# Kernel tuning notes

Measured on AMD Instinct MI355X. Metric: run time of the kernel, lower is better.

The kernel has to match this reference:

```python
import jax, jax.numpy as jnp
import numpy as np

B, NO, NR, D = 128, 256, 512, 1024


def setup_inputs() -> dict:
    key = jax.random.key(0)
    ks = jax.random.split(key, 8)
    obj_vecs = jax.random.normal(ks[0], (B, NO, D), dtype=jnp.float32)
    attr_vecs = jax.random.normal(ks[1], (B, NO, D), dtype=jnp.float32)
    rela_vecs = jax.random.normal(ks[2], (B, NR, D), dtype=jnp.float32)
    edges = jax.random.randint(ks[3], (B, NR, 2), 0, NO, dtype=jnp.int64)
    rela_masks = jnp.ones((B, NR, 1), dtype=jnp.float32)
    # Linear params (torch Linear: y = x @ W.T + b); store as [in, out]
    sa = 1.0 / np.sqrt(2 * D)
    sr = 1.0 / np.sqrt(3 * D)
    W_attr = jax.random.uniform(ks[4], (2 * D, D), jnp.float32, -sa, sa)
    b_attr = jax.random.uniform(ks[5], (D,), jnp.float32, -sa, sa)
    W_rela = jax.random.uniform(ks[6], (3 * D, D), jnp.float32, -sr, sr)
    b_rela = jax.random.uniform(ks[7], (D,), jnp.float32, -sr, sr)
    return {"obj_vecs": obj_vecs, "attr_vecs": attr_vecs, "rela_vecs": rela_vecs,
            "edges": edges, "rela_masks": rela_masks,
            "W_attr": W_attr, "b_attr": b_attr, "W_rela": W_rela, "b_rela": b_rela}


def reference(obj_vecs, attr_vecs, rela_vecs, edges, rela_masks,
              W_attr, b_attr, W_rela, b_rela):
    b, no, d = obj_vecs.shape
    nr = rela_vecs.shape[1]
    # feat_3d_to_2d: flatten batch, offset edge indices into the flat object table
    obj2 = obj_vecs.reshape(b * no, d)
    attr2 = attr_vecs.reshape(b * no, d)
    rela2 = rela_vecs.reshape(b * nr, d)
    offs = (jnp.arange(b, dtype=edges.dtype) * no)[:, None, None]  # [b,1,1]
    e2 = (edges + offs).reshape(b * nr, 2)

    # attribute branch: Linear(ReLU) on cat[obj, attr] + residual (dropout = eval/no-op)
    new_attr = jax.nn.relu(jnp.concatenate([obj2, attr2], axis=-1) @ W_attr + b_attr) + attr2

    # relation branch (rela_gnn_type == 0): gather subject/object, cat[s, rela, o]
    s_vecs = obj2[e2[:, 0]]  # [b*nr, d]
    o_vecs = obj2[e2[:, 1]]
    t_vecs = jnp.concatenate([s_vecs, rela2, o_vecs], axis=-1)  # [b*nr, 3d]
    new_rela = jax.nn.relu(t_vecs @ W_rela + b_rela) + rela2

    # feat_2d_to_3d: reshape back and apply relation mask
    new_obj3 = obj_vecs
    new_attr3 = new_attr.reshape(b, no, d)
    new_rela3 = new_rela.reshape(b, nr, d) * rela_masks
    return (new_obj3, new_attr3, new_rela3)
```

## Files before the change

kernel.cpp:

```cpp
#include <hip/hip_runtime.h>

#define B_   128
#define NO_  256
#define NR_  512
#define D_   1024

typedef __bf16 bf16x8 __attribute__((ext_vector_type(8)));
typedef float  f32x4  __attribute__((ext_vector_type(4)));

__device__ __forceinline__ unsigned short f2b(float f){
  unsigned int u = __float_as_uint(f);
  unsigned int r = (u + 0x7fffu + ((u >> 16) & 1u)) >> 16;
  return (unsigned short)r;
}

__global__ void conv_f32_bf16(const float4* __restrict__ in, uint4* __restrict__ out, int n8){
  int i = blockIdx.x * blockDim.x + threadIdx.x;
  if (i >= n8) return;
  float4 a = in[2*i], b = in[2*i+1];
  union { unsigned short s[8]; uint4 v; } p;
  p.s[0]=f2b(a.x); p.s[1]=f2b(a.y); p.s[2]=f2b(a.z); p.s[3]=f2b(a.w);
  p.s[4]=f2b(b.x); p.s[5]=f2b(b.y); p.s[6]=f2b(b.z); p.s[7]=f2b(b.w);
  out[i] = p.v;
}

__global__ void copy_vec4(const uint4* __restrict__ in, uint4* __restrict__ out, int n){
  int i = blockIdx.x * blockDim.x + threadIdx.x;
  if (i < n) out[i] = in[i];
}

__global__ void transpose_f32_bf16(const float* __restrict__ in,
                                   unsigned short* __restrict__ out, int R, int C){
  __shared__ unsigned short tile[32][33];
  int tx = threadIdx.x, ty = threadIdx.y;
  int x  = blockIdx.x * 32 + tx;
  int y0 = blockIdx.y * 32;
  #pragma unroll
  for (int i = 0; i < 4; i++) tile[ty + i*8][tx] = f2b(in[(size_t)(y0 + ty + i*8) * C + x]);
  __syncthreads();
  int ox  = y0 + tx;
  int oy0 = blockIdx.x * 32;
  #pragma unroll
  for (int i = 0; i < 4; i++) out[(size_t)(oy0 + ty + i*8) * R + ox] = tile[tx][ty + i*8];
}

template<int MODE>
__global__ void gemm_fused(const unsigned short* __restrict__ objb,
                           const unsigned short* __restrict__ xresb,
                           const float* __restrict__ xresf,
                           const int* __restrict__ edges,
                           const float* __restrict__ mask,
                           const unsigned short* __restrict__ WT,
                           const float* __restrict__ bias,
                           float* __restrict__ out)
{
  constexpr int K   = MODE ? 3*D_ : 2*D_;
  constexpr int LDA = 72;
  __shared__ unsigned short Asm[128*LDA];
  __shared__ unsigned short Bsm[128*LDA];

  const int t  = threadIdx.x;
  const int l  = t & 63;
  const int w  = t >> 6;
  const int wr = w >> 1, wc = w & 1;
  const int m0 = blockIdx.y * 128;
  const int n0 = blockIdx.x * 128;

  const int sr = t >> 3;
  const int sc = (t & 7) * 8;

  const unsigned short* pA0[4];
  const unsigned short* pA1[4];
  const unsigned short* pA2[4];
  #pragma unroll
  for (int i = 0; i < 4; i++){
    int m = m0 + i*32 + sr;
    if (MODE == 0){
      pA0[i] = objb  + (size_t)m * D_;
      pA1[i] = xresb + (size_t)m * D_;
      pA2[i] = nullptr;
    } else {
      int b = m >> 9;
      int s = edges[2*m];
      int o = edges[2*m + 1];
      pA0[i] = objb  + (size_t)((b << 8) + s) * D_;
      pA1[i] = xresb + (size_t)m * D_;
      pA2[i] = objb  + (size_t)((b << 8) + o) * D_;
    }
  }
  const unsigned short* pB[4];
  #pragma unroll
  for (int i = 0; i < 4; i++) pB[i] = WT + (size_t)(n0 + i*32 + sr) * K;

  f32x4 acc[4][4];
  #pragma unroll
  for (int x = 0; x < 4; x++)
    #pragma unroll
    for (int y = 0; y < 4; y++) acc[x][y] = (f32x4){0.f,0.f,0.f,0.f};

  const int kq = (l >> 4) * 8;
  const int fr = l & 15;

  for (int k0 = 0; k0 < K; k0 += 64){
    #pragma unroll
    for (int i = 0; i < 4; i++){
      const unsigned short* ga;
      if (MODE == 0){
        ga = (k0 < D_) ? pA0[i] + k0 : pA1[i] + (k0 - D_);
      } else {
        ga = (k0 < D_)   ? pA0[i] + k0
           : (k0 < 2*D_) ? pA1[i] + (k0 - D_)
           :               pA2[i] + (k0 - 2*D_);
      }
      *(uint4*)&Asm[(i*32 + sr) * LDA + sc] = *(const uint4*)(ga + sc);
      *(uint4*)&Bsm[(i*32 + sr) * LDA + sc] = *(const uint4*)(pB[i] + k0 + sc);
    }
    __syncthreads();

    #pragma unroll
    for (int ks = 0; ks < 2; ks++){
      bf16x8 af[4], bfv[4];
      #pragma unroll
      for (int x = 0; x < 4; x++)
        af[x]  = *(const bf16x8*)&Asm[(wr*64 + x*16 + fr) * LDA + ks*32 + kq];
      #pragma unroll
      for (int y = 0; y < 4; y++)
        bfv[y] = *(const bf16x8*)&Bsm[(wc*64 + y*16 + fr) * LDA + ks*32 + kq];
      #pragma unroll
      for (int x = 0; x < 4; x++)
        #pragma unroll
        for (int y = 0; y < 4; y++)
          acc[x][y] = __builtin_amdgcn_mfma_f32_16x16x32_bf16(af[x], bfv[y], acc[x][y], 0, 0, 0);
    }
    __syncthreads();
  }

  const int colb = n0 + wc*64 + fr;
  float bv[4];
  #pragma unroll
  for (int y = 0; y < 4; y++) bv[y] = bias[colb + y*16];

  const int rowb = m0 + wr*64 + ((l >> 4) << 2);
  #pragma unroll
  for (int x = 0; x < 4; x++){
    #pragma unroll
    for (int i = 0; i < 4; i++){
      int gr = rowb + x*16 + i;
      float mk = 1.f;
      if (MODE == 1) mk = mask[gr];
      size_t rbase = (size_t)gr * D_;
      #pragma unroll
      for (int y = 0; y < 4; y++){
        int gc = colb + y*16;
        float v = acc[x][y][i] + bv[y];
        v = fmaxf(v, 0.f) + xresf[rbase + gc];
        if (MODE == 1) v *= mk;
        out[rbase + gc] = v;
      }
    }
  }
}

extern "C" void kernel_launch(void* const* d_in, const int* in_sizes, int n_in,
                              void* d_out, int out_size, void* d_ws, size_t ws_size,
                              hipStream_t stream){
  const float* obj   = (const float*)d_in[0];
  const float* attr  = (const float*)d_in[1];
  const float* rela  = (const float*)d_in[2];
  const int*   edges = (const int*)d_in[3];
  const float* masks = (const float*)d_in[4];
  const float* Wa    = (const float*)d_in[5];
  const float* ba    = (const float*)d_in[6];
  const float* Wr    = (const float*)d_in[7];
  const float* br    = (const float*)d_in[8];

  const size_t NOBJ  = (size_t)B_*NO_*D_;
  const size_t NRELA = (size_t)B_*NR_*D_;

  float* out0 = (float*)d_out;
  float* out1 = out0 + NOBJ;
  float* out2 = out1 + NOBJ;

  unsigned short* objb  = (unsigned short*)d_out;
  unsigned short* attrb = objb + NOBJ;
  unsigned short* relab = (unsigned short*)(out1);
  unsigned short* WTa = (unsigned short*)d_ws;
  unsigned short* WTr = WTa + (size_t)1024*2048;

  conv_f32_bf16<<<(int)(NOBJ/8/256),  256, 0, stream>>>((const float4*)obj,  (uint4*)objb,  (int)(NOBJ/8));
  conv_f32_bf16<<<(int)(NOBJ/8/256),  256, 0, stream>>>((const float4*)attr, (uint4*)attrb, (int)(NOBJ/8));
  conv_f32_bf16<<<(int)(NRELA/8/256), 256, 0, stream>>>((const float4*)rela, (uint4*)relab, (int)(NRELA/8));

  transpose_f32_bf16<<<dim3(1024/32, 2048/32), dim3(32,8), 0, stream>>>(Wa, WTa, 2048, 1024);
  transpose_f32_bf16<<<dim3(1024/32, 3072/32), dim3(32,8), 0, stream>>>(Wr, WTr, 3072, 1024);

  gemm_fused<1><<<dim3(8, (B_*NR_)/128), 256, 0, stream>>>(objb, relab, rela, edges, masks, WTr, br, out2);
  gemm_fused<0><<<dim3(8, (B_*NO_)/128), 256, 0, stream>>>(objb, attrb, attr, nullptr, nullptr, WTa, ba, out1);

  int nv = (int)(NOBJ / 4);
  copy_vec4<<<nv/256, 256, 0, stream>>>((const uint4*)obj, (uint4*)out0, nv);
}
```

Measured before the change: 1.677 ms.

## Rewrite fused GEMM with 256x256 tiles, direct-to-LDS loads and double buffering

Measured after the change: 1.462 ms. 1.15x faster.

```diff
diff --git a/kernel.cpp b/kernel.cpp
--- a/kernel.cpp
+++ b/kernel.cpp
@@ -44,115 +44,181 @@
   for (int i = 0; i < 4; i++) out[(size_t)(oy0 + ty + i*8) * R + ox] = tile[tx][ty + i*8];
 }
 
+__device__ __forceinline__ void gload16(const void* g, void* l){
+  __builtin_amdgcn_global_load_lds((const __attribute__((address_space(1))) void*)g,
+                                   (__attribute__((address_space(3))) void*)l,
+                                   16, 0, 0);
+}
+
 template<int MODE>
-__global__ void gemm_fused(const unsigned short* __restrict__ objb,
-                           const unsigned short* __restrict__ xresb,
-                           const float* __restrict__ xresf,
-                           const int* __restrict__ edges,
-                           const float* __restrict__ mask,
-                           const unsigned short* __restrict__ WT,
-                           const float* __restrict__ bias,
-                           float* __restrict__ out)
+__global__ __launch_bounds__(512, 2)
+void gemm_fused(const unsigned short* __restrict__ objb,
+                const unsigned short* __restrict__ xresb,
+                const float* __restrict__ xresf,
+                const int* __restrict__ edges,
+                const float* __restrict__ mask,
+                const unsigned short* __restrict__ WT,
+                const float* __restrict__ bias,
+                float* __restrict__ out)
 {
-  constexpr int K   = MODE ? 3*D_ : 2*D_;
-  constexpr int LDA = 72;
-  __shared__ unsigned short Asm[128*LDA];
-  __shared__ unsigned short Bsm[128*LDA];
+  constexpr int K  = MODE ? 3*D_ : 2*D_;
+  constexpr int NT = K / 64;
+
+  __shared__ unsigned short Asm[2][2][128*64];
+  __shared__ unsigned short Bsm[2][2][128*64];
 
   const int t  = threadIdx.x;
   const int l  = t & 63;
   const int w  = t >> 6;
-  const int wr = w >> 1, wc = w & 1;
-  const int m0 = blockIdx.y * 128;
-  const int n0 = blockIdx.x * 128;
-
-  const int sr = t >> 3;
-  const int sc = (t & 7) * 8;
-
-  const unsigned short* pA0[4];
-  const unsigned short* pA1[4];
-  const unsigned short* pA2[4];
-  #pragma unroll
-  for (int i = 0; i < 4; i++){
-    int m = m0 + i*32 + sr;
-    if (MODE == 0){
-      pA0[i] = objb  + (size_t)m * D_;
-      pA1[i] = xresb + (size_t)m * D_;
-      pA2[i] = nullptr;
-    } else {
-      int b = m >> 9;
-      int s = edges[2*m];
-      int o = edges[2*m + 1];
-      pA0[i] = objb  + (size_t)((b << 8) + s) * D_;
-      pA1[i] = xresb + (size_t)m * D_;
-      pA2[i] = objb  + (size_t)((b << 8) + o) * D_;
+  const int wr = w >> 2;
+  const int wc = w & 3;
+
+  const int q8  = gridDim.x >> 3;
+  const int lin = (blockIdx.x & 7) * q8 + (blockIdx.x >> 3);
+  const int m0  = (lin >> 2) * 256;
+  const int n0  = (lin & 3) * 256;
+
+  const int trow = t >> 3;
+  const int gsl  = (((t & 7) ^ (trow & 7)) << 3);
+
+  unsigned int offA0[4], offA1[4], offA2[4], offB[4];
+  #pragma unroll
+  for (int h = 0; h < 2; h++){
+    #pragma unroll
+    for (int r = 0; r < 2; r++){
+      const int hr = h*2 + r;
+      const int m  = m0 + h*128 + r*64 + trow;
+      if (MODE == 0){
+        offA0[hr] = (unsigned)m * D_ + gsl;
+        offA1[hr] = offA0[hr];
+        offA2[hr] = 0;
+      } else {
+        const int b = m >> 9;
+        const int s = edges[2*m], o = edges[2*m+1];
+        offA0[hr] = (unsigned)((b << 8) + s) * D_ + gsl;
+        offA1[hr] = (unsigned)m * D_ + gsl;
+        offA2[hr] = (unsigned)((b << 8) + o) * D_ + gsl;
+      }
+      const int n = n0 + h*128 + r*64 + trow;
+      offB[hr] = (unsigned)n * K + gsl;
     }
   }
-  const unsigned short* pB[4];
-  #pragma unroll
-  for (int i = 0; i < 4; i++) pB[i] = WT + (size_t)(n0 + i*32 + sr) * K;
-
-  f32x4 acc[4][4];
-  #pragma unroll
-  for (int x = 0; x < 4; x++)
-    #pragma unroll
-    for (int y = 0; y < 4; y++) acc[x][y] = (f32x4){0.f,0.f,0.f,0.f};
-
-  const int kq = (l >> 4) * 8;
-  const int fr = l & 15;
-
-  for (int k0 = 0; k0 < K; k0 += 64){
-    #pragma unroll
-    for (int i = 0; i < 4; i++){
-      const unsigned short* ga;
-      if (MODE == 0){
-        ga = (k0 < D_) ? pA0[i] + k0 : pA1[i] + (k0 - D_);
-      } else {
-        ga = (k0 < D_)   ? pA0[i] + k0
-           : (k0 < 2*D_) ? pA1[i] + (k0 - D_)
-           :               pA2[i] + (k0 - 2*D_);
-      }
-      *(uint4*)&Asm[(i*32 + sr) * LDA + sc] = *(const uint4*)(ga + sc);
-      *(uint4*)&Bsm[(i*32 + sr) * LDA + sc] = *(const uint4*)(pB[i] + k0 + sc);
-    }
-    __syncthreads();
-
-    #pragma unroll
-    for (int ks = 0; ks < 2; ks++){
-      bf16x8 af[4], bfv[4];
-      #pragma unroll
-      for (int x = 0; x < 4; x++)
-        af[x]  = *(const bf16x8*)&Asm[(wr*64 + x*16 + fr) * LDA + ks*32 + kq];
-      #pragma unroll
-      for (int y = 0; y < 4; y++)
-        bfv[y] = *(const bf16x8*)&Bsm[(wc*64 + y*16 + fr) * LDA + ks*32 + kq];
-      #pragma unroll
-      for (int x = 0; x < 4; x++)
-        #pragma unroll
-        for (int y = 0; y < 4; y++)
-          acc[x][y] = __builtin_amdgcn_mfma_f32_16x16x32_bf16(af[x], bfv[y], acc[x][y], 0, 0, 0);
-    }
-    __syncthreads();
+
+#define STAGE_A(tile, half) do{                                               \
+    const int _tl = (tile); const int _k = _tl*64; const int _b = _tl & 1;    \
+    const unsigned short *_g0, *_g1;                                          \
+    if (MODE == 0){                                                           \
+      if (_k < D_){ _g0 = objb  + offA0[(half)*2+0] + _k;                     \
+                    _g1 = objb  + offA0[(half)*2+1] + _k; }                   \
+      else        { _g0 = xresb + offA1[(half)*2+0] + (_k - D_);              \
+                    _g1 = xresb + offA1[(half)*2+1] + (_k - D_); }            \
+    } else {                                                                  \
+      if (_k < D_){ _g0 = objb  + offA0[(half)*2+0] + _k;                     \
+                    _g1 = objb  + offA0[(half)*2+1] + _k; }                   \
+      else if (_k < 2*D_){ _g0 = xresb + offA1[(half)*2+0] + (_k - D_);       \
+                           _g1 = xresb + offA1[(half)*2+1] + (_k - D_); }     \
+      else        { _g0 = objb  + offA2[(half)*2+0] + (_k - 2*D_);            \
+                    _g1 = objb  + offA2[(half)*2+1] + (_k - 2*D_); }          \
+    }                                                                         \
+    gload16(_g0, &Asm[_b][half][(w*8     ) * 64]);                            \
+    gload16(_g1, &Asm[_b][half][(w*8 + 64) * 64]);                            \
+  }while(0)
+
+#define STAGE_B(tile, half) do{                                               \
+    const int _tl = (tile); const int _k = _tl*64; const int _b = _tl & 1;    \
+    gload16(WT + offB[(half)*2+0] + _k, &Bsm[_b][half][(w*8     ) * 64]);     \
+    gload16(WT + offB[(half)*2+1] + _k, &Bsm[_b][half][(w*8 + 64) * 64]);     \
+  }while(0)
+
+  f32x4 acc[8][4];
+  #pragma unroll
+  for (int X = 0; X < 8; X++)
+    #pragma unroll
+    for (int Y = 0; Y < 4; Y++) acc[X][Y] = (f32x4){0.f,0.f,0.f,0.f};
+
+  const int fr  = l & 15;
+  const int swz = (fr & 7) << 4;
+  const int rdo = (l >> 4) << 4;
+
+  auto lda = [&](int buf, int qm, int x, int kh) -> bf16x8 {
+    const int r = qm*64 + x*16 + fr;
+    return *(const bf16x8*)((const char*)&Asm[buf][wr][r*64] + ((kh*64 + rdo) ^ swz));
+  };
+  auto ldb = [&](int buf, int qn, int y, int kh) -> bf16x8 {
+    const int r = (wc & 1)*64 + qn*32 + y*16 + fr;
+    return *(const bf16x8*)((const char*)&Bsm[buf][wc>>1][r*64] + ((kh*64 + rdo) ^ swz));
+  };
+
+  bf16x8 af[4][2], bq0[2][2], bq1[2][2];
+
+#define MFMA16(qm, qn, BQ)                                                    \
+  __builtin_amdgcn_s_setprio(1);                                              \
+  _Pragma("unroll")                                                           \
+  for (int x = 0; x < 4; x++){                                                \
+    _Pragma("unroll")                                                         \
+    for (int y = 0; y < 2; y++){                                              \
+      acc[(qm)*4+x][(qn)*2+y] = __builtin_amdgcn_mfma_f32_16x16x32_bf16(      \
+          af[x][0], BQ[y][0], acc[(qm)*4+x][(qn)*2+y], 0, 0, 0);              \
+      acc[(qm)*4+x][(qn)*2+y] = __builtin_amdgcn_mfma_f32_16x16x32_bf16(      \
+          af[x][1], BQ[y][1], acc[(qm)*4+x][(qn)*2+y], 0, 0, 0);              \
+    }                                                                         \
+  }                                                                           \
+  __builtin_amdgcn_s_setprio(0);
+
+  STAGE_A(0,0); STAGE_A(0,1); STAGE_B(0,0); STAGE_B(0,1);
+  STAGE_A(1,0);
+  asm volatile("s_waitcnt vmcnt(2)" ::: "memory");
+  __builtin_amdgcn_s_barrier();
+
+  for (int tt = 0; tt < NT; ++tt){
+    const int cur = tt & 1;
+    #pragma unroll
+    for (int x = 0; x < 4; x++){ af[x][0] = lda(cur,0,x,0); af[x][1] = lda(cur,0,x,1); }
+    #pragma unroll
+    for (int y = 0; y < 2; y++){ bq0[y][0] = ldb(cur,0,y,0); bq0[y][1] = ldb(cur,0,y,1); }
+    if (tt+1 < NT) STAGE_A(tt+1, 1);
+    __builtin_amdgcn_s_barrier();
+    MFMA16(0,0,bq0)
+    __builtin_amdgcn_s_barrier();
+    #pragma unroll
+    for (int y = 0; y < 2; y++){ bq1[y][0] = ldb(cur,1,y,0); bq1[y][1] = ldb(cur,1,y,1); }
+    if (tt+1 < NT) STAGE_B(tt+1, 0);
+    __builtin_amdgcn_s_barrier();
+    MFMA16(0,1,bq1)
+    __builtin_amdgcn_s_barrier();
+    #pragma unroll
+    for (int x = 0; x < 4; x++){ af[x][0] = lda(cur,1,x,0); af[x][1] = lda(cur,1,x,1); }
+    if (tt+1 < NT) STAGE_B(tt+1, 1);
+    __builtin_amdgcn_s_barrier();
+    MFMA16(1,1,bq1)
+    __builtin_amdgcn_s_barrier();
+    if (tt+2 < NT) STAGE_A(tt+2, 0);
+    MFMA16(1,0,bq0)
+    asm volatile("s_waitcnt vmcnt(2)" ::: "memory");
+    __builtin_amdgcn_s_barrier();
   }
+#undef STAGE_A
+#undef STAGE_B
+#undef MFMA16
 
   const int colb = n0 + wc*64 + fr;
   float bv[4];
   #pragma unroll
-  for (int y = 0; y < 4; y++) bv[y] = bias[colb + y*16];
-
-  const int rowb = m0 + wr*64 + ((l >> 4) << 2);
-  #pragma unroll
-  for (int x = 0; x < 4; x++){
+  for (int Y = 0; Y < 4; Y++) bv[Y] = bias[colb + Y*16];
+
+  const int rowq = (l >> 4) << 2;
+  #pragma unroll
+  for (int X = 0; X < 8; X++){
     #pragma unroll
     for (int i = 0; i < 4; i++){
-      int gr = rowb + x*16 + i;
+      const int gr = m0 + wr*128 + X*16 + rowq + i;
       float mk = 1.f;
       if (MODE == 1) mk = mask[gr];
-      size_t rbase = (size_t)gr * D_;
+      const size_t rbase = (size_t)gr * D_;
       #pragma unroll
-      for (int y = 0; y < 4; y++){
-        int gc = colb + y*16;
-        float v = acc[x][y][i] + bv[y];
+      for (int Y = 0; Y < 4; Y++){
+        const int gc = colb + Y*16;
+        float v = acc[X][Y][i] + bv[Y];
         v = fmaxf(v, 0.f) + xresf[rbase + gc];
         if (MODE == 1) v *= mk;
         out[rbase + gc] = v;
@@ -194,8 +260,8 @@
   transpose_f32_bf16<<<dim3(1024/32, 2048/32), dim3(32,8), 0, stream>>>(Wa, WTa, 2048, 1024);
   transpose_f32_bf16<<<dim3(1024/32, 3072/32), dim3(32,8), 0, stream>>>(Wr, WTr, 3072, 1024);
 
-  gemm_fused<1><<<dim3(8, (B_*NR_)/128), 256, 0, stream>>>(objb, relab, rela, edges, masks, WTr, br, out2);
-  gemm_fused<0><<<dim3(8, (B_*NO_)/128), 256, 0, stream>>>(objb, attrb, attr, nullptr, nullptr, WTa, ba, out1);
+  gemm_fused<1><<<(B_*NR_/256)*(D_/256), 512, 0, stream>>>(objb, relab, rela, edges, masks, WTr, br, out2);
+  gemm_fused<0><<<(B_*NO_/256)*(D_/256), 512, 0, stream>>>(objb, attrb, attr, nullptr, nullptr, WTa, ba, out1);
 
   int nv = (int)(NOBJ / 4);
   copy_vec4<<<nv/256, 256, 0, stream>>>((const uint4*)obj, (uint4*)out0, nv);
```
